# Kernel optimization log

Hardware: AMD Instinct MI355X
Metric: run time of the kernel (lower is better)

Reference implementation:

```python
import jax, jax.numpy as jnp
import numpy as np

T, B, IN, OUT, N_MOD, K = 1024, 8, 1024, 1024, 16, 2

def setup_inputs() -> dict:
    key = jax.random.key(0)
    k1, k2, k3, k4 = jax.random.split(key, 4)
    x = jax.random.normal(k1, (T, B, IN), dtype=jnp.float32)
    selection = jax.random.randint(k2, (B, K), 0, N_MOD, dtype=jnp.int64)
    weight = jax.random.normal(k3, (N_MOD, IN, OUT), dtype=jnp.float32) * (1.0 / np.sqrt(IN))
    bias = jax.random.normal(k4, (N_MOD, OUT), dtype=jnp.float32) * 0.02
    return {"x": x, "selection": selection, "weight": weight, "bias": bias}

def reference(x, selection, weight, bias):
    # time_major=True: x is [T, B, in] -> batch-major [B, T, in]
    xb = jnp.swapaxes(x, 0, 1)
    # Gather the K selected expert weight matrices per batch row: [B, K, in, out]
    W_sel = weight[selection]
    # Equivalent to matmul(x[i], cat(weight[sel], dim=1)): [B, T, K, out]
    o = jnp.einsum('bti,bkio->btko', xb, W_sel)
    Bn, Tn, Kn, On = o.shape
    o = o.reshape(Bn, Tn, Kn * On)
    # concat_dim == 1 bias: bias[sel].view(1, -1) -> [1, K*out], broadcast over T
    o = o + bias[selection].reshape(Bn, 1, Kn * On)
    # back to time-major [T, B, K*out]
    return jnp.swapaxes(o, 0, 1)
```

## Files before the change

### kernel.cpp

```cpp
#include <hip/hip_runtime.h>

#define T_DIM 1024
#define B_DIM 8
#define IN_DIM 1024
#define OUT_DIM 1024
#define N_MODL 16
#define K_SEL 2

typedef unsigned short ushort_t;
typedef __bf16 bf16x8 __attribute__((ext_vector_type(8)));
typedef float f32x4 __attribute__((ext_vector_type(4)));

__device__ __forceinline__ unsigned int f2bf2(float lo, float hi) {
  union { float f; unsigned int u; } a, b; a.f = lo; b.f = hi;
  unsigned int ra = (a.u + 0x7fffu + ((a.u >> 16) & 1u)) >> 16;
  unsigned int rb = (b.u + 0x7fffu + ((b.u >> 16) & 1u)) >> 16;
  return ra | (rb << 16);
}

__device__ __forceinline__ void async_g2l(const void* g, void* l) {
  __builtin_amdgcn_global_load_lds(
      (const __attribute__((address_space(1))) unsigned int*)g,
      (__attribute__((address_space(3))) unsigned int*)l,
      16, 0, 0);
}

__device__ __forceinline__ int read_sel(const int* __restrict__ s, int g) {
  bool i64 = true;
#pragma unroll
  for (int j = 0; j < 8; ++j) i64 &= (s[2 * j + 1] == 0);
  return i64 ? s[2 * g] : s[g];
}

__global__ __launch_bounds__(256) void convert_kernel(const float* __restrict__ x,
                                                      const float* __restrict__ w,
                                                      const int* __restrict__ selp,
                                                      ushort_t* __restrict__ xb,
                                                      ushort_t* __restrict__ wt) {
  __shared__ ushort_t tb[128 * 128];
  const int bid = blockIdx.x;
  if (bid >= 1024) {
    const int i = (bid - 1024) * 256 + threadIdx.x;
    const float4* s = (const float4*)x;
    float4 a = s[i * 2], b = s[i * 2 + 1];
    uint4 o;
    o.x = f2bf2(a.x, a.y); o.y = f2bf2(a.z, a.w);
    o.z = f2bf2(b.x, b.y); o.w = f2bf2(b.z, b.w);
    ((uint4*)xb)[i] = o;
    return;
  }
  const int m = bid >> 6;
  bool used = false;
#pragma unroll
  for (int g = 0; g < B_DIM * K_SEL; ++g) used |= (read_sel(selp, g) == m);
  if (!used) return;

  const int i0 = ((bid >> 3) & 7) * 128;
  const int o0 = (bid & 7) * 128;
  const float* src = w + ((size_t)(m * IN_DIM + i0)) * OUT_DIM + o0;

  const int o4 = (threadIdx.x & 31) * 4;
  const int ib = threadIdx.x >> 5;
#pragma unroll
  for (int p = 0; p < 16; ++p) {
    const int i = ib + p * 8;
    float4 v = *(const float4*)(src + (size_t)i * OUT_DIM + o4);
    const int osw = o4 ^ (((i >> 3) & 15) << 2);
    uint2 d2; d2.x = f2bf2(v.x, v.y); d2.y = f2bf2(v.z, v.w);
    *(uint2*)(tb + i * 128 + osw) = d2;
  }
  __syncthreads();

  ushort_t* dst = wt + ((size_t)(m * OUT_DIM + o0)) * IN_DIM + i0;
  const int il = (threadIdx.x & 15) * 8;
  const int ob = threadIdx.x >> 4;
  const int q2 = ((il >> 3) & 15) << 2;
#pragma unroll
  for (int p = 0; p < 8; ++p) {
    const int o = ob + p * 16;
    const int osw = o ^ q2;
    uint4 d;
    unsigned int u[8];
#pragma unroll
    for (int j = 0; j < 8; ++j) u[j] = tb[(il + j) * 128 + osw];
    d.x = u[0] | (u[1] << 16); d.y = u[2] | (u[3] << 16);
    d.z = u[4] | (u[5] << 16); d.w = u[6] | (u[7] << 16);
    *(uint4*)(dst + (size_t)o * IN_DIM + il) = d;
  }
}

#define MFMA16 __builtin_amdgcn_mfma_f32_16x16x32_bf16

template<bool LAST>
__device__ __forceinline__ void gstep(
    int t, const ushort_t* curB0, const ushort_t* curB1,
    ushort_t* nxtB0, ushort_t* nxtB1,
    const ushort_t* Ag, const ushort_t* Bb0, const ushort_t* Bb1,
    int wv, int brdo, int cb,
    f32x4 (&acc0)[4][4], f32x4 (&acc1)[4][4]) {
  const int k0 = t * 64;
  bf16x8 af0[4], af1[4];
#pragma unroll
  for (int i = 0; i < 4; ++i) {
    const ushort_t* ap = Ag + (size_t)i * 16 * (B_DIM * IN_DIM) + k0;
    af0[i] = *(const bf16x8*)(ap);
    af1[i] = *(const bf16x8*)(ap + 32);
  }
  __builtin_amdgcn_sched_barrier(0);
  if (!LAST) {
    const int k1 = k0 + 64;
#pragma unroll
    for (int c = 0; c < 4; ++c) {
      const int j = wv * 4 + c;
      async_g2l(Bb0 + (size_t)8 * j * IN_DIM + k1, nxtB0 + j * 512);
      async_g2l(Bb1 + (size_t)8 * j * IN_DIM + k1, nxtB1 + j * 512);
    }
    __builtin_amdgcn_sched_barrier(0);
  }
  const ushort_t* Brd0 = curB0 + brdo;
  const ushort_t* Brd1 = curB1 + brdo;
#pragma unroll
  for (int kk = 0; kk < 2; ++kk) {
    const int co = kk ? (cb ^ 32) : cb;
    bf16x8 b0[4], b1[4];
#pragma unroll
    for (int n = 0; n < 4; ++n) {
      b0[n] = *(const bf16x8*)(Brd0 + n * 1024 + co);
      b1[n] = *(const bf16x8*)(Brd1 + n * 1024 + co);
    }
    const bf16x8* afp = kk ? af1 : af0;
#pragma unroll
    for (int mt = 0; mt < 4; ++mt)
#pragma unroll
      for (int nt = 0; nt < 4; ++nt) {
        acc0[mt][nt] = MFMA16(afp[mt], b0[nt], acc0[mt][nt], 0, 0, 0);
        acc1[mt][nt] = MFMA16(afp[mt], b1[nt], acc1[mt][nt], 0, 0, 0);
      }
  }
  if (!LAST) {
    __builtin_amdgcn_sched_barrier(0);
    asm volatile("s_waitcnt vmcnt(0)" ::: "memory");
    __builtin_amdgcn_sched_barrier(0);
    __builtin_amdgcn_s_barrier();
    __builtin_amdgcn_sched_barrier(0);
  }
}

__global__ __launch_bounds__(256, 2) void mlgemm_kernel(const ushort_t* __restrict__ xb,
                                                        const ushort_t* __restrict__ wt,
                                                        const int* __restrict__ selp,
                                                        const float* __restrict__ bias,
                                                        float* __restrict__ out) {
  __shared__ ushort_t Bs[2][2][128 * 64];

  const int lin = blockIdx.x;
  const int b = lin & 7;
  const int mtile = (lin >> 3) & 7;
  const int ntile = lin >> 6;
  const int e0 = read_sel(selp, 2 * b);
  const int e1 = read_sel(selp, 2 * b + 1);
  const int m0 = mtile * 128;
  const int n0 = ntile * 128;

  const int lane = threadIdx.x & 63;
  const int wv = threadIdx.x >> 6;

  const int srow = lane >> 3;
  const int sx = (((lane & 7) ^ (srow & 7)) << 3);
  const ushort_t* Bb0 = wt + ((size_t)(e0 * OUT_DIM + n0 + srow)) * IN_DIM + sx;
  const ushort_t* Bb1 = wt + ((size_t)(e1 * OUT_DIM + n0 + srow)) * IN_DIM + sx;

  const int frow = lane & 15;
  const int quad = lane >> 4;
  const int cb = ((quad ^ (frow & 7)) << 3);
  const int wrow = (wv & 1) * 64;
  const int wcol = (wv >> 1) * 64;
  const int brdo = (wcol + frow) * 64;

  const ushort_t* Ag = xb + (size_t)(m0 + wrow + frow) * (B_DIM * IN_DIM)
                          + b * IN_DIM + quad * 8;

  f32x4 acc0[4][4] = {};
  f32x4 acc1[4][4] = {};

#pragma unroll
  for (int c = 0; c < 4; ++c) {
    const int j = wv * 4 + c;
    async_g2l(Bb0 + (size_t)8 * j * IN_DIM, Bs[0][0] + j * 512);
    async_g2l(Bb1 + (size_t)8 * j * IN_DIM, Bs[0][1] + j * 512);
  }
  __builtin_amdgcn_sched_barrier(0);
  asm volatile("s_waitcnt vmcnt(0)" ::: "memory");
  __builtin_amdgcn_sched_barrier(0);
  __builtin_amdgcn_s_barrier();
  __builtin_amdgcn_sched_barrier(0);

  for (int t = 0; t < 14; t += 2) {
    gstep<false>(t,     Bs[0][0], Bs[0][1], Bs[1][0], Bs[1][1],
                 Ag, Bb0, Bb1, wv, brdo, cb, acc0, acc1);
    gstep<false>(t + 1, Bs[1][0], Bs[1][1], Bs[0][0], Bs[0][1],
                 Ag, Bb0, Bb1, wv, brdo, cb, acc0, acc1);
  }
  gstep<false>(14, Bs[0][0], Bs[0][1], Bs[1][0], Bs[1][1],
               Ag, Bb0, Bb1, wv, brdo, cb, acc0, acc1);
  gstep<true>(15, Bs[1][0], Bs[1][1], Bs[0][0], Bs[0][1],
              Ag, Bb0, Bb1, wv, brdo, cb, acc0, acc1);

  const int orow0 = m0 + wrow + quad * 4;
  const int ocol0 = n0 + wcol + frow;
  const float* bp0 = bias + (size_t)e0 * OUT_DIM;
  const float* bp1 = bias + (size_t)e1 * OUT_DIM;
  float bv0[4], bv1[4];
#pragma unroll
  for (int nt = 0; nt < 4; ++nt) {
    bv0[nt] = bp0[ocol0 + nt * 16];
    bv1[nt] = bp1[ocol0 + nt * 16];
  }
  float* C0 = out + (size_t)b * (K_SEL * OUT_DIM);
  float* C1 = C0 + OUT_DIM;
#pragma unroll
  for (int mt = 0; mt < 4; ++mt) {
#pragma unroll
    for (int r = 0; r < 4; ++r) {
      const size_t rowoff = (size_t)(orow0 + mt * 16 + r) * (B_DIM * K_SEL * OUT_DIM);
#pragma unroll
      for (int nt = 0; nt < 4; ++nt) {
        C0[rowoff + ocol0 + nt * 16] = acc0[mt][nt][r] + bv0[nt];
        C1[rowoff + ocol0 + nt * 16] = acc1[mt][nt][r] + bv1[nt];
      }
    }
  }
}

extern "C" void kernel_launch(void* const* d_in, const int* in_sizes, int n_in,
                              void* d_out, int out_size, void* d_ws, size_t ws_size,
                              hipStream_t stream) {
  const float* x    = (const float*)d_in[0];
  const int*   sel  = (const int*)d_in[1];
  const float* w    = (const float*)d_in[2];
  const float* bias = (const float*)d_in[3];
  float* out = (float*)d_out;

  ushort_t* xb = (ushort_t*)d_ws;
  ushort_t* wt = (ushort_t*)((char*)d_ws +
                             (size_t)T_DIM * B_DIM * IN_DIM * 2);

  convert_kernel<<<dim3(1024 + T_DIM * B_DIM * IN_DIM / 8 / 256), 256, 0, stream>>>(
      x, w, sel, xb, wt);
  mlgemm_kernel<<<dim3(8 * 8 * B_DIM), 256, 0, stream>>>(xb, wt, sel, bias, out);
}
```

Before: 189.1 us.

## Stage A tiles in LDS, halve N tile, double grid size

```diff
diff --git a/kernel.cpp b/kernel.cpp
--- a/kernel.cpp
+++ b/kernel.cpp
@@ -91,67 +91,13 @@
 
 #define MFMA16 __builtin_amdgcn_mfma_f32_16x16x32_bf16
 
-template<bool LAST>
-__device__ __forceinline__ void gstep(
-    int t, const ushort_t* curB0, const ushort_t* curB1,
-    ushort_t* nxtB0, ushort_t* nxtB1,
-    const ushort_t* Ag, const ushort_t* Bb0, const ushort_t* Bb1,
-    int wv, int brdo, int cb,
-    f32x4 (&acc0)[4][4], f32x4 (&acc1)[4][4]) {
-  const int k0 = t * 64;
-  bf16x8 af0[4], af1[4];
-#pragma unroll
-  for (int i = 0; i < 4; ++i) {
-    const ushort_t* ap = Ag + (size_t)i * 16 * (B_DIM * IN_DIM) + k0;
-    af0[i] = *(const bf16x8*)(ap);
-    af1[i] = *(const bf16x8*)(ap + 32);
-  }
-  __builtin_amdgcn_sched_barrier(0);
-  if (!LAST) {
-    const int k1 = k0 + 64;
-#pragma unroll
-    for (int c = 0; c < 4; ++c) {
-      const int j = wv * 4 + c;
-      async_g2l(Bb0 + (size_t)8 * j * IN_DIM + k1, nxtB0 + j * 512);
-      async_g2l(Bb1 + (size_t)8 * j * IN_DIM + k1, nxtB1 + j * 512);
-    }
-    __builtin_amdgcn_sched_barrier(0);
-  }
-  const ushort_t* Brd0 = curB0 + brdo;
-  const ushort_t* Brd1 = curB1 + brdo;
-#pragma unroll
-  for (int kk = 0; kk < 2; ++kk) {
-    const int co = kk ? (cb ^ 32) : cb;
-    bf16x8 b0[4], b1[4];
-#pragma unroll
-    for (int n = 0; n < 4; ++n) {
-      b0[n] = *(const bf16x8*)(Brd0 + n * 1024 + co);
-      b1[n] = *(const bf16x8*)(Brd1 + n * 1024 + co);
-    }
-    const bf16x8* afp = kk ? af1 : af0;
-#pragma unroll
-    for (int mt = 0; mt < 4; ++mt)
-#pragma unroll
-      for (int nt = 0; nt < 4; ++nt) {
-        acc0[mt][nt] = MFMA16(afp[mt], b0[nt], acc0[mt][nt], 0, 0, 0);
-        acc1[mt][nt] = MFMA16(afp[mt], b1[nt], acc1[mt][nt], 0, 0, 0);
-      }
-  }
-  if (!LAST) {
-    __builtin_amdgcn_sched_barrier(0);
-    asm volatile("s_waitcnt vmcnt(0)" ::: "memory");
-    __builtin_amdgcn_sched_barrier(0);
-    __builtin_amdgcn_s_barrier();
-    __builtin_amdgcn_sched_barrier(0);
-  }
-}
-
 __global__ __launch_bounds__(256, 2) void mlgemm_kernel(const ushort_t* __restrict__ xb,
                                                         const ushort_t* __restrict__ wt,
                                                         const int* __restrict__ selp,
                                                         const float* __restrict__ bias,
                                                         float* __restrict__ out) {
-  __shared__ ushort_t Bs[2][2][128 * 64];
+  __shared__ ushort_t As[2][128 * 64];
+  __shared__ ushort_t Bs[2][2][64 * 64];
 
   const int lin = blockIdx.x;
   const int b = lin & 7;
@@ -160,13 +106,14 @@
   const int e0 = read_sel(selp, 2 * b);
   const int e1 = read_sel(selp, 2 * b + 1);
   const int m0 = mtile * 128;
-  const int n0 = ntile * 128;
+  const int n0 = ntile * 64;
 
   const int lane = threadIdx.x & 63;
   const int wv = threadIdx.x >> 6;
 
   const int srow = lane >> 3;
   const int sx = (((lane & 7) ^ (srow & 7)) << 3);
+  const ushort_t* Ab  = xb + (size_t)(m0 + srow) * (B_DIM * IN_DIM) + b * IN_DIM + sx;
   const ushort_t* Bb0 = wt + ((size_t)(e0 * OUT_DIM + n0 + srow)) * IN_DIM + sx;
   const ushort_t* Bb1 = wt + ((size_t)(e1 * OUT_DIM + n0 + srow)) * IN_DIM + sx;
 
@@ -174,45 +121,82 @@
   const int quad = lane >> 4;
   const int cb = ((quad ^ (frow & 7)) << 3);
   const int wrow = (wv & 1) * 64;
-  const int wcol = (wv >> 1) * 64;
+  const int wcol = (wv >> 1) * 32;
+  const int ardo = (wrow + frow) * 64;
   const int brdo = (wcol + frow) * 64;
 
-  const ushort_t* Ag = xb + (size_t)(m0 + wrow + frow) * (B_DIM * IN_DIM)
-                          + b * IN_DIM + quad * 8;
-
-  f32x4 acc0[4][4] = {};
-  f32x4 acc1[4][4] = {};
+  f32x4 acc0[4][2] = {};
+  f32x4 acc1[4][2] = {};
 
 #pragma unroll
   for (int c = 0; c < 4; ++c) {
     const int j = wv * 4 + c;
+    async_g2l(Ab + (size_t)8 * j * (B_DIM * IN_DIM), As[0] + j * 512);
+  }
+#pragma unroll
+  for (int c = 0; c < 2; ++c) {
+    const int j = wv * 2 + c;
     async_g2l(Bb0 + (size_t)8 * j * IN_DIM, Bs[0][0] + j * 512);
     async_g2l(Bb1 + (size_t)8 * j * IN_DIM, Bs[0][1] + j * 512);
   }
-  __builtin_amdgcn_sched_barrier(0);
-  asm volatile("s_waitcnt vmcnt(0)" ::: "memory");
-  __builtin_amdgcn_sched_barrier(0);
-  __builtin_amdgcn_s_barrier();
-  __builtin_amdgcn_sched_barrier(0);
-
-  for (int t = 0; t < 14; t += 2) {
-    gstep<false>(t,     Bs[0][0], Bs[0][1], Bs[1][0], Bs[1][1],
-                 Ag, Bb0, Bb1, wv, brdo, cb, acc0, acc1);
-    gstep<false>(t + 1, Bs[1][0], Bs[1][1], Bs[0][0], Bs[0][1],
-                 Ag, Bb0, Bb1, wv, brdo, cb, acc0, acc1);
-  }
-  gstep<false>(14, Bs[0][0], Bs[0][1], Bs[1][0], Bs[1][1],
-               Ag, Bb0, Bb1, wv, brdo, cb, acc0, acc1);
-  gstep<true>(15, Bs[1][0], Bs[1][1], Bs[0][0], Bs[0][1],
-              Ag, Bb0, Bb1, wv, brdo, cb, acc0, acc1);
+
+#pragma unroll
+  for (int t = 0; t < 16; ++t) {
+    const int cur = t & 1;
+    __builtin_amdgcn_sched_barrier(0);
+    asm volatile("s_waitcnt vmcnt(0)" ::: "memory");
+    __builtin_amdgcn_sched_barrier(0);
+    __builtin_amdgcn_s_barrier();
+    __builtin_amdgcn_sched_barrier(0);
+    if (t < 15) {
+      const int k1 = (t + 1) * 64;
+      const int nxt = cur ^ 1;
+#pragma unroll
+      for (int c = 0; c < 4; ++c) {
+        const int j = wv * 4 + c;
+        async_g2l(Ab + (size_t)8 * j * (B_DIM * IN_DIM) + k1, As[nxt] + j * 512);
+      }
+#pragma unroll
+      for (int c = 0; c < 2; ++c) {
+        const int j = wv * 2 + c;
+        async_g2l(Bb0 + (size_t)8 * j * IN_DIM + k1, Bs[nxt][0] + j * 512);
+        async_g2l(Bb1 + (size_t)8 * j * IN_DIM + k1, Bs[nxt][1] + j * 512);
+      }
+      __builtin_amdgcn_sched_barrier(0);
+    }
+    const ushort_t* Ard  = As[cur] + ardo;
+    const ushort_t* Brd0 = Bs[cur][0] + brdo;
+    const ushort_t* Brd1 = Bs[cur][1] + brdo;
+#pragma unroll
+    for (int kk = 0; kk < 2; ++kk) {
+      const int co = kk ? (cb ^ 32) : cb;
+      bf16x8 af[4], b0[2], b1[2];
+#pragma unroll
+      for (int i = 0; i < 4; ++i) af[i] = *(const bf16x8*)(Ard + i * 1024 + co);
+#pragma unroll
+      for (int n = 0; n < 2; ++n) {
+        b0[n] = *(const bf16x8*)(Brd0 + n * 1024 + co);
+        b1[n] = *(const bf16x8*)(Brd1 + n * 1024 + co);
+      }
+      __builtin_amdgcn_s_setprio(1);
+#pragma unroll
+      for (int mt = 0; mt < 4; ++mt)
+#pragma unroll
+        for (int nt = 0; nt < 2; ++nt) {
+          acc0[mt][nt] = MFMA16(af[mt], b0[nt], acc0[mt][nt], 0, 0, 0);
+          acc1[mt][nt] = MFMA16(af[mt], b1[nt], acc1[mt][nt], 0, 0, 0);
+        }
+      __builtin_amdgcn_s_setprio(0);
+    }
+  }
 
   const int orow0 = m0 + wrow + quad * 4;
   const int ocol0 = n0 + wcol + frow;
   const float* bp0 = bias + (size_t)e0 * OUT_DIM;
   const float* bp1 = bias + (size_t)e1 * OUT_DIM;
-  float bv0[4], bv1[4];
-#pragma unroll
-  for (int nt = 0; nt < 4; ++nt) {
+  float bv0[2], bv1[2];
+#pragma unroll
+  for (int nt = 0; nt < 2; ++nt) {
     bv0[nt] = bp0[ocol0 + nt * 16];
     bv1[nt] = bp1[ocol0 + nt * 16];
   }
@@ -224,7 +208,7 @@
     for (int r = 0; r < 4; ++r) {
       const size_t rowoff = (size_t)(orow0 + mt * 16 + r) * (B_DIM * K_SEL * OUT_DIM);
 #pragma unroll
-      for (int nt = 0; nt < 4; ++nt) {
+      for (int nt = 0; nt < 2; ++nt) {
         C0[rowoff + ocol0 + nt * 16] = acc0[mt][nt][r] + bv0[nt];
         C1[rowoff + ocol0 + nt * 16] = acc1[mt][nt][r] + bv1[nt];
       }
@@ -247,5 +231,5 @@
 
   convert_kernel<<<dim3(1024 + T_DIM * B_DIM * IN_DIM / 8 / 256), 256, 0, stream>>>(
       x, w, sel, xb, wt);
-  mlgemm_kernel<<<dim3(8 * 8 * B_DIM), 256, 0, stream>>>(xb, wt, sel, bias, out);
-}
+  mlgemm_kernel<<<dim3(8 * 8 * 16), 256, 0, stream>>>(xb, wt, sel, bias, out);
+}
```

Result: faster. 182.5 us (-3.5%).
